# Performance work log

Hardware: AMD Instinct MI355X
Metric: run time of the kernel (lower is better)

## Reference

```python
import jax, jax.numpy as jnp
import numpy as np

N = 100000      # nodes
E = 1600000     # edges (avg degree 16)
F_IN = 64       # input features
HID = 16        # ChebConv hidden (fixed in source)
C = 40          # num_classes
K = 2           # Chebyshev order (fixed in source)
LAMBDA_MAX = 2.0  # PyG ChebConv default


def setup_inputs() -> dict:
    key = jax.random.key(0)
    ks = jax.random.split(key, 6)
    x = jax.random.normal(ks[0], (N, F_IN), dtype=jnp.float32)
    edge_index = jax.random.randint(ks[1], (2, E), 0, N, dtype=jnp.int32)
    edge_weight = jax.random.uniform(ks[2], (E,), dtype=jnp.float32)
    W1 = jax.random.normal(ks[3], (K, F_IN, HID), dtype=jnp.float32) / np.float32(np.sqrt(F_IN))
    b1 = jnp.zeros((HID,), dtype=jnp.float32)
    W2 = jax.random.normal(ks[4], (K, HID, C), dtype=jnp.float32) / np.float32(np.sqrt(HID))
    b2 = jnp.zeros((C,), dtype=jnp.float32)
    return {"x": x, "edge_weight": edge_weight, "W1": W1, "b1": b1,
            "W2": W2, "b2": b2, "edge_index": edge_index}


def _cheb_norm(src, dst, edge_weight):
    # deg from symmetric normalization (aggregate at dst, PyG col)
    deg = jax.ops.segment_sum(edge_weight, dst, num_segments=N)
    dinv = jnp.where(deg > 0, jax.lax.rsqrt(jnp.maximum(deg, 1e-30)), 0.0)
    # Lhat = 2L/lambda_max - I ; with L = I - A_norm -> edge weight = -(2/lmax)*A_norm
    norm = -(2.0 / LAMBDA_MAX) * dinv[src] * edge_weight * dinv[dst]
    loop = 2.0 / LAMBDA_MAX - 1.0  # self-loop weight (0 for lambda_max=2)
    return norm, loop


def _cheb_conv(x, src, dst, norm, loop, W, b):
    # K=2: Tx0 = x, Tx1 = Lhat @ x (sparse gather-scale-scatter)
    Tx1 = jax.ops.segment_sum(norm[:, None] * x[src], dst, num_segments=N) + loop * x
    return jnp.einsum('nf,fo->no', x, W[0]) + jnp.einsum('nf,fo->no', Tx1, W[1]) + b


def reference(x, edge_weight, W1, b1, W2, b2, edge_index):
    src, dst = edge_index[0], edge_index[1]
    norm, loop = _cheb_norm(src, dst, edge_weight)
    h = jax.nn.relu(_cheb_conv(x, src, dst, norm, loop, W1, b1))
    # F.dropout with training=False is identity (inference reference)
    o = _cheb_conv(h, src, dst, norm, loop, W2, b2)
    return jax.nn.log_softmax(o, axis=1)
```

## Files before the change

### kernel.cpp

```cpp
#include <hip/hip_runtime.h>
#include <math.h>

#define NN 100000
#define NE 1600000
#define FIN 64
#define HID 16
#define NC 40

#define NG 512
#define GN 196
#define GCAP 3600
#define CH 4096
#define NBK ((NE + CH - 1) / CH)

typedef unsigned int u32;
typedef unsigned long long u64;
typedef unsigned short u16;

__device__ inline u16 f2bf(float f) {
    u32 u = __float_as_uint(f);
    return (u16)((u + 0x7FFF + ((u >> 16) & 1)) >> 16);
}
__device__ inline float bf2f(u16 v) { return __uint_as_float(((u32)v) << 16); }

__global__ void k_zero(int* __restrict__ p) {
    p[blockIdx.x * 256 + threadIdx.x] = 0;
}

__global__ void __launch_bounds__(256) k_bucket(const int* __restrict__ src,
                                                const int* __restrict__ dst,
                                                const float* __restrict__ ew,
                                                int* __restrict__ bcur,
                                                u64* __restrict__ stg) {
    __shared__ u64 stage[CH];
    __shared__ int lcnt[NG];
    __shared__ int loff[NG];
    __shared__ int lcur[NG];
    __shared__ int gst[NG];
    __shared__ int ssum[256];
    __shared__ int totsh;
    int tid = threadIdx.x;
    int e0 = blockIdx.x * CH;
    for (int i = tid; i < NG; i += 256) lcnt[i] = 0;
    __syncthreads();
    u32 hb[16];
    #pragma unroll
    for (int k = 0; k < 16; ++k) {
        int e = e0 + k * 256 + tid;
        hb[k] = 0xFFFFFFFFu;
        if (e < NE) {
            int d = dst[e];
            int g = d / GN;
            hb[k] = ((u32)g << 16) | (u32)(d - g * GN);
            atomicAdd(&lcnt[g], 1);
        }
    }
    __syncthreads();
    int b0 = lcnt[2 * tid], b1c = lcnt[2 * tid + 1];
    int s = b0 + b1c;
    ssum[tid] = s;
    __syncthreads();
    #pragma unroll
    for (int off = 1; off < 256; off <<= 1) {
        int t = tid >= off ? ssum[tid - off] : 0;
        __syncthreads();
        ssum[tid] += t;
        __syncthreads();
    }
    int excl = ssum[tid] - s;
    loff[2 * tid] = excl;         loff[2 * tid + 1] = excl + b0;
    lcur[2 * tid] = excl;         lcur[2 * tid + 1] = excl + b0;
    gst[2 * tid]     = atomicAdd(&bcur[(2 * tid) << 4], b0);
    gst[2 * tid + 1] = atomicAdd(&bcur[(2 * tid + 1) << 4], b1c);
    if (tid == 255) totsh = ssum[255];
    __syncthreads();
    #pragma unroll
    for (int k = 0; k < 16; ++k) {
        if (hb[k] != 0xFFFFFFFFu) {
            int e = e0 + k * 256 + tid;
            int g = hb[k] >> 16;
            u32 q = (u32)fminf(ew[e] * 32767.f + 0.5f, 32767.f);
            u32 lo = (u32)src[e] | (q << 17);
            int slot = atomicAdd(&lcur[g], 1);
            stage[slot] = ((u64)hb[k] << 32) | (u64)lo;
        }
    }
    __syncthreads();
    int total = totsh;
    for (int i = tid; i < total; i += 256) {
        u64 r = stage[i];
        int g = (int)(r >> 48);
        int slot = gst[g] + (i - loff[g]);
        if (slot < GCAP) stg[(size_t)g * GCAP + slot] = r;
    }
}

__global__ void __launch_bounds__(256) k_build(const u64* __restrict__ stg,
                                               const int* __restrict__ bcur,
                                               int* __restrict__ row_ptr,
                                               float* __restrict__ dinv,
                                               u32* __restrict__ edges4) {
    __shared__ u32 hc[GN];
    __shared__ u32 hw[GN];
    __shared__ int tsum[256];
    __shared__ int sb[NG];
    int g = blockIdx.x, tid = threadIdx.x;
    for (int i = tid; i < GN; i += 256) { hc[i] = 0; hw[i] = 0; }
    for (int i = tid; i < NG; i += 256) sb[i] = bcur[i << 4];
    __syncthreads();
    int n = sb[g];
    int b0 = sb[2 * tid], b1 = sb[2 * tid + 1];
    const u64* base = stg + (size_t)g * GCAP;
    for (int i = tid; i < n; i += 256) {
        u64 r = base[i];
        int ld = (int)((r >> 32) & 0xFFFF);
        atomicAdd(&hc[ld], 1u);
        atomicAdd(&hw[ld], ((u32)r) >> 17);
    }
    __syncthreads();
    int s2 = b0 + b1;
    tsum[tid] = s2;
    __syncthreads();
    #pragma unroll
    for (int off = 1; off < 256; off <<= 1) {
        int t = tid >= off ? tsum[tid - off] : 0;
        __syncthreads();
        tsum[tid] += t;
        __syncthreads();
    }
    int excl = tsum[tid] - s2;
    sb[2 * tid] = excl; sb[2 * tid + 1] = excl + b0;
    __syncthreads();
    int gbase = sb[g];
    int c = (tid < GN) ? (int)hc[tid] : 0;
    tsum[tid] = c;
    __syncthreads();
    #pragma unroll
    for (int off = 1; off < 256; off <<= 1) {
        int t = tid >= off ? tsum[tid - off] : 0;
        __syncthreads();
        tsum[tid] += t;
        __syncthreads();
    }
    if (tid < GN) {
        int run = gbase + tsum[tid] - c;
        int nd = g * GN + tid;
        if (nd <= NN) {
            row_ptr[nd] = run;
            if (nd < NN) {
                float deg = (float)hw[tid] * (1.0f / 32767.0f);
                dinv[nd] = deg > 0.f ? rsqrtf(fmaxf(deg, 1e-30f)) : 0.f;
            }
        }
        hc[tid] = (u32)run;
    }
    __syncthreads();
    for (int i = tid; i < n; i += 256) {
        u64 r = base[i];
        int ld = (int)((r >> 32) & 0xFFFF);
        edges4[atomicAdd(&hc[ld], 1u)] = (u32)r;
    }
}

__global__ void __launch_bounds__(256) k_mm1(const float* __restrict__ x,
                                             const float* __restrict__ W1,
                                             const float* __restrict__ dinv,
                                             float* __restrict__ A1,
                                             u16* __restrict__ B0h) {
    __shared__ float4 w4[512];
    int tid = threadIdx.x;
    for (int i = tid; i < 512; i += 256) w4[i] = *(const float4*)(W1 + i * 4);
    __syncthreads();
    int sel = tid >> 7;
    int node = blockIdx.x * 128 + (tid & 127);
    if (node >= NN) return;
    const float4* xr = (const float4*)(x + node * FIN);
    const float4* wb = w4 + sel * 256;
    float4 a0 = {0,0,0,0}, a1 = {0,0,0,0}, a2 = {0,0,0,0}, a3 = {0,0,0,0};
    #pragma unroll
    for (int ft = 0; ft < 16; ++ft) {
        float4 xv = xr[ft];
        const float4* wf = wb + ft * 16;
        #pragma unroll
        for (int q = 0; q < 4; ++q) {
            float xs = q == 0 ? xv.x : q == 1 ? xv.y : q == 2 ? xv.z : xv.w;
            float4 w0 = wf[q * 4 + 0], w1v = wf[q * 4 + 1], w2v = wf[q * 4 + 2], w3v = wf[q * 4 + 3];
            a0.x += xs * w0.x; a0.y += xs * w0.y; a0.z += xs * w0.z; a0.w += xs * w0.w;
            a1.x += xs * w1v.x; a1.y += xs * w1v.y; a1.z += xs * w1v.z; a1.w += xs * w1v.w;
            a2.x += xs * w2v.x; a2.y += xs * w2v.y; a2.z += xs * w2v.z; a2.w += xs * w2v.w;
            a3.x += xs * w3v.x; a3.y += xs * w3v.y; a3.z += xs * w3v.z; a3.w += xs * w3v.w;
        }
    }
    if (sel == 0) {
        float4* o = (float4*)(A1 + node * HID);
        o[0] = a0; o[1] = a1; o[2] = a2; o[3] = a3;
    } else {
        float di = dinv[node];
        uint4 p0, p1;
        p0.x = f2bf(a0.x * di) | ((u32)f2bf(a0.y * di) << 16);
        p0.y = f2bf(a0.z * di) | ((u32)f2bf(a0.w * di) << 16);
        p0.z = f2bf(a1.x * di) | ((u32)f2bf(a1.y * di) << 16);
        p0.w = f2bf(a1.z * di) | ((u32)f2bf(a1.w * di) << 16);
        p1.x = f2bf(a2.x * di) | ((u32)f2bf(a2.y * di) << 16);
        p1.y = f2bf(a2.z * di) | ((u32)f2bf(a2.w * di) << 16);
        p1.z = f2bf(a3.x * di) | ((u32)f2bf(a3.y * di) << 16);
        p1.w = f2bf(a3.z * di) | ((u32)f2bf(a3.w * di) << 16);
        uint4* o = (uint4*)(B0h + node * HID);
        o[0] = p0; o[1] = p1;
    }
}

template <int MODE>
__global__ void k_gather(const int* __restrict__ row_ptr, const u32* __restrict__ edges4,
                         const u16* __restrict__ Bh,
                         const float* __restrict__ A1, const float* __restrict__ b1,
                         const float* __restrict__ dinv,
                         float* __restrict__ o1, u16* __restrict__ o2) {
    int node = blockIdx.x * 4 + (threadIdx.x >> 6);
    int lane = threadIdx.x & 63;
    int es = lane >> 4, j = lane & 15;
    if (node >= NN) return;
    int beg = row_ptr[node], end = row_ptr[node + 1];
    int p0 = beg + es;
    float acc = 0.f;
    if (end - beg <= 16) {
        u32 r[4];
        #pragma unroll
        for (int k = 0; k < 4; ++k) {
            int p = p0 + 4 * k;
            r[k] = (p < end) ? edges4[p] : 0u;
        }
        #pragma unroll
        for (int k = 0; k < 4; ++k)
            acc += (float)(r[k] >> 17) * bf2f(Bh[(r[k] & 0x1FFFF) * HID + j]);
    } else {
        u32 r[8];
        #pragma unroll
        for (int k = 0; k < 8; ++k) {
            int p = p0 + 4 * k;
            r[k] = (p < end) ? edges4[p] : 0u;
        }
        #pragma unroll
        for (int k = 0; k < 8; ++k)
            acc += (float)(r[k] >> 17) * bf2f(Bh[(r[k] & 0x1FFFF) * HID + j]);
        for (int p = p0 + 32; p < end; p += 4) {
            u32 rr = edges4[p];
            acc += (float)(rr >> 17) * bf2f(Bh[(rr & 0x1FFFF) * HID + j]);
        }
    }
    acc *= (1.0f / 32767.0f);
    acc += __shfl_xor(acc, 16, 64);
    acc += __shfl_xor(acc, 32, 64);
    if (es == 0) {
        float di = dinv[node];
        if (MODE == 0) {
            float v = A1[node * HID + j] - di * acc + b1[j];
            float hh = fmaxf(v, 0.f);
            o1[node * HID + j] = hh;
            o2[node * HID + j] = f2bf(hh * di);
        } else {
            o1[node * HID + j] = -di * acc;
        }
    }
}

__global__ void __launch_bounds__(256) k_mm2_lsm(const float* __restrict__ h,
                                                 const float* __restrict__ Th,
                                                 const float* __restrict__ W2,
                                                 const float* __restrict__ b2,
                                                 float* __restrict__ out) {
    __shared__ float4 w4[32][10];
    __shared__ float sb2[NC];
    int tid = threadIdx.x;
    for (int i = tid; i < 320; i += 256) {
        int f = i / 10, ct = i % 10;
        w4[f][ct] = *(const float4*)(W2 + f * 40 + ct * 4);
    }
    for (int i = tid; i < NC; i += 256) sb2[i] = b2[i];
    __syncthreads();
    int node = blockIdx.x * 256 + tid;
    if (node >= NN) return;
    float v[32];
    const float4* hp = (const float4*)(h + node * HID);
    const float4* tp = (const float4*)(Th + node * HID);
    #pragma unroll
    for (int q = 0; q < 4; ++q) {
        float4 a = hp[q];
        v[4 * q + 0] = a.x; v[4 * q + 1] = a.y; v[4 * q + 2] = a.z; v[4 * q + 3] = a.w;
        float4 b = tp[q];
        v[16 + 4 * q + 0] = b.x; v[16 + 4 * q + 1] = b.y; v[16 + 4 * q + 2] = b.z; v[16 + 4 * q + 3] = b.w;
    }
    float lg[NC];
    #pragma unroll
    for (int ct = 0; ct < 10; ++ct) {
        float ax = sb2[ct * 4 + 0], ay = sb2[ct * 4 + 1], az = sb2[ct * 4 + 2], aw = sb2[ct * 4 + 3];
        #pragma unroll
        for (int f = 0; f < 32; ++f) {
            float4 wv = w4[f][ct];
            ax += v[f] * wv.x; ay += v[f] * wv.y; az += v[f] * wv.z; aw += v[f] * wv.w;
        }
        lg[ct * 4 + 0] = ax; lg[ct * 4 + 1] = ay; lg[ct * 4 + 2] = az; lg[ct * 4 + 3] = aw;
    }
    float m = lg[0];
    #pragma unroll
    for (int c = 1; c < NC; ++c) m = fmaxf(m, lg[c]);
    float sum = 0.f;
    #pragma unroll
    for (int c = 0; c < NC; ++c) sum += __expf(lg[c] - m);
    float lse = m + __logf(sum);
    float* orow = out + node * NC;
    #pragma unroll
    for (int ct = 0; ct < 10; ++ct) {
        float4 r;
        r.x = lg[ct * 4 + 0] - lse; r.y = lg[ct * 4 + 1] - lse;
        r.z = lg[ct * 4 + 2] - lse; r.w = lg[ct * 4 + 3] - lse;
        *(float4*)(orow + ct * 4) = r;
    }
}

extern "C" void kernel_launch(void* const* d_in, const int* in_sizes, int n_in,
                              void* d_out, int out_size, void* d_ws, size_t ws_size,
                              hipStream_t stream) {
    const float* x  = (const float*)d_in[0];
    const float* ew = (const float*)d_in[1];
    const float* W1 = (const float*)d_in[2];
    const float* b1 = (const float*)d_in[3];
    const float* W2 = (const float*)d_in[4];
    const float* b2 = (const float*)d_in[5];
    const int*   ei = (const int*)d_in[6];
    const int* src = ei;
    const int* dst = ei + NE;
    float* out = (float*)d_out;

    const int NPAD = 100352;
    int*   bcur    = (int*)d_ws;
    u64*   stg     = (u64*)(bcur + NG * 16);
    u32*   edges4  = (u32*)(stg + (size_t)NG * GCAP);
    int*   row_ptr = (int*)(edges4 + NE);
    float* dinv    = (float*)(row_ptr + NPAD);
    float* A1      = dinv + NPAD;
    float* h       = A1 + NN * HID;
    float* Th      = h + NN * HID;
    u16*   B0h     = (u16*)(Th + NN * HID);
    u16*   h2      = B0h + NN * HID;

    k_zero<<<NG * 16 / 256, 256, 0, stream>>>(bcur);
    k_bucket<<<NBK, 256, 0, stream>>>(src, dst, ew, bcur, stg);
    k_build<<<NG, 256, 0, stream>>>(stg, bcur, row_ptr, dinv, edges4);
    k_mm1<<<(NN + 127) / 128, 256, 0, stream>>>(x, W1, dinv, A1, B0h);
    k_gather<0><<<(NN + 3) / 4, 256, 0, stream>>>(row_ptr, edges4, B0h, A1, b1, dinv, h, h2);
    k_gather<1><<<(NN + 3) / 4, 256, 0, stream>>>(row_ptr, edges4, h2, nullptr, nullptr, dinv, Th, nullptr);
    k_mm2_lsm<<<(NN + 255) / 256, 256, 0, stream>>>(h, Th, W2, b2, out);
}
```

Measured before the change: 135.1 us.

## Rewrite SpMM gather as edge-parallel blocks with shared-memory atomic accumulation

The CSR gather kernels change from one wavefront per node to one block per 64-node group. Threads now iterate over all edges of the group, eight threads per edge with each loading a packed bf16 pair, and accumulate into shared memory with atomics keyed by a new per-edge local destination byte. The build kernel writes that byte. The aim is to balance load across nodes of uneven degree and remove idle lanes on low-degree nodes. The cost is an extra byte array written and read per edge, plus shared-memory atomic contention among edges that share a destination.

```diff
diff --git a/kernel.cpp b/kernel.cpp
--- a/kernel.cpp
+++ b/kernel.cpp
@@ -12,16 +12,18 @@
 #define GCAP 3600
 #define CH 4096
 #define NBK ((NE + CH - 1) / CH)
+#define GB 64
+#define NGB ((NN + GB - 1) / GB)
 
 typedef unsigned int u32;
 typedef unsigned long long u64;
 typedef unsigned short u16;
+typedef unsigned char u8;
 
 __device__ inline u16 f2bf(float f) {
     u32 u = __float_as_uint(f);
     return (u16)((u + 0x7FFF + ((u >> 16) & 1)) >> 16);
 }
-__device__ inline float bf2f(u16 v) { return __uint_as_float(((u32)v) << 16); }
 
 __global__ void k_zero(int* __restrict__ p) {
     p[blockIdx.x * 256 + threadIdx.x] = 0;
@@ -99,7 +101,8 @@
                                                const int* __restrict__ bcur,
                                                int* __restrict__ row_ptr,
                                                float* __restrict__ dinv,
-                                               u32* __restrict__ edges4) {
+                                               u32* __restrict__ edges4,
+                                               u8* __restrict__ dloc) {
     __shared__ u32 hc[GN];
     __shared__ u32 hw[GN];
     __shared__ int tsum[256];
@@ -158,7 +161,9 @@
     for (int i = tid; i < n; i += 256) {
         u64 r = base[i];
         int ld = (int)((r >> 32) & 0xFFFF);
-        edges4[atomicAdd(&hc[ld], 1u)] = (u32)r;
+        int pos = (int)atomicAdd(&hc[ld], 1u);
+        edges4[pos] = (u32)r;
+        dloc[pos] = (u8)((g * GN + ld) & 63);
     }
 }
 
@@ -211,55 +216,54 @@
 }
 
 template <int MODE>
-__global__ void k_gather(const int* __restrict__ row_ptr, const u32* __restrict__ edges4,
-                         const u16* __restrict__ Bh,
-                         const float* __restrict__ A1, const float* __restrict__ b1,
-                         const float* __restrict__ dinv,
-                         float* __restrict__ o1, u16* __restrict__ o2) {
-    int node = blockIdx.x * 4 + (threadIdx.x >> 6);
-    int lane = threadIdx.x & 63;
-    int es = lane >> 4, j = lane & 15;
-    if (node >= NN) return;
-    int beg = row_ptr[node], end = row_ptr[node + 1];
-    int p0 = beg + es;
-    float acc = 0.f;
-    if (end - beg <= 16) {
-        u32 r[4];
-        #pragma unroll
-        for (int k = 0; k < 4; ++k) {
-            int p = p0 + 4 * k;
-            r[k] = (p < end) ? edges4[p] : 0u;
-        }
-        #pragma unroll
-        for (int k = 0; k < 4; ++k)
-            acc += (float)(r[k] >> 17) * bf2f(Bh[(r[k] & 0x1FFFF) * HID + j]);
-    } else {
-        u32 r[8];
-        #pragma unroll
-        for (int k = 0; k < 8; ++k) {
-            int p = p0 + 4 * k;
-            r[k] = (p < end) ? edges4[p] : 0u;
-        }
-        #pragma unroll
-        for (int k = 0; k < 8; ++k)
-            acc += (float)(r[k] >> 17) * bf2f(Bh[(r[k] & 0x1FFFF) * HID + j]);
-        for (int p = p0 + 32; p < end; p += 4) {
-            u32 rr = edges4[p];
-            acc += (float)(rr >> 17) * bf2f(Bh[(rr & 0x1FFFF) * HID + j]);
-        }
-    }
-    acc *= (1.0f / 32767.0f);
-    acc += __shfl_xor(acc, 16, 64);
-    acc += __shfl_xor(acc, 32, 64);
-    if (es == 0) {
-        float di = dinv[node];
+__global__ void __launch_bounds__(256) k_gather(const int* __restrict__ row_ptr,
+                                                const u32* __restrict__ edges4,
+                                                const u8* __restrict__ dloc,
+                                                const u16* __restrict__ Bh,
+                                                const float* __restrict__ A1,
+                                                const float* __restrict__ b1,
+                                                const float* __restrict__ dinv,
+                                                float* __restrict__ o1,
+                                                u16* __restrict__ o2) {
+    __shared__ float acc[GB * HID];
+    int tid = threadIdx.x;
+    int n0 = blockIdx.x * GB;
+    #pragma unroll
+    for (int i = tid; i < GB * HID; i += 256) acc[i] = 0.f;
+    __syncthreads();
+    int nend = n0 + GB; if (nend > NN) nend = NN;
+    int beg = row_ptr[n0], end = row_ptr[nend];
+    const u32* Bw = (const u32*)Bh;
+    int total = (end - beg) << 3;
+    for (int i = tid; i < total; i += 256) {
+        int e = beg + (i >> 3);
+        int q = i & 7;
+        u32 rec = edges4[e];
+        u32 c = Bw[(rec & 0x1FFFF) * 8 + q];
+        float w = (float)(rec >> 17);
+        int dl = (int)dloc[e];
+        atomicAdd(&acc[dl * HID + 2 * q],     w * __uint_as_float(c << 16));
+        atomicAdd(&acc[dl * HID + 2 * q + 1], w * __uint_as_float(c & 0xFFFF0000u));
+    }
+    __syncthreads();
+    for (int idx = tid; idx < GB * 8; idx += 256) {
+        int ln = idx >> 3, q = idx & 7;
+        int nd = n0 + ln;
+        if (nd >= NN) continue;
+        float di = dinv[nd];
+        float sc = di * (1.0f / 32767.0f);
+        float aL = acc[ln * HID + 2 * q];
+        float aH = acc[ln * HID + 2 * q + 1];
+        int f = 2 * q;
         if (MODE == 0) {
-            float v = A1[node * HID + j] - di * acc + b1[j];
-            float hh = fmaxf(v, 0.f);
-            o1[node * HID + j] = hh;
-            o2[node * HID + j] = f2bf(hh * di);
+            float2 a = *(const float2*)(A1 + nd * HID + f);
+            float2 bb = *(const float2*)(b1 + f);
+            float hL = fmaxf(a.x - sc * aL + bb.x, 0.f);
+            float hH = fmaxf(a.y - sc * aH + bb.y, 0.f);
+            *(float2*)(o1 + nd * HID + f) = make_float2(hL, hH);
+            ((u32*)o2)[nd * 8 + q] = (u32)f2bf(hL * di) | ((u32)f2bf(hH * di) << 16);
         } else {
-            o1[node * HID + j] = -di * acc;
+            *(float2*)(o1 + nd * HID + f) = make_float2(-sc * aL, -sc * aH);
         }
     }
 }
@@ -343,12 +347,13 @@
     float* Th      = h + NN * HID;
     u16*   B0h     = (u16*)(Th + NN * HID);
     u16*   h2      = B0h + NN * HID;
+    u8*    dloc    = (u8*)(h2 + NN * HID);
 
     k_zero<<<NG * 16 / 256, 256, 0, stream>>>(bcur);
     k_bucket<<<NBK, 256, 0, stream>>>(src, dst, ew, bcur, stg);
-    k_build<<<NG, 256, 0, stream>>>(stg, bcur, row_ptr, dinv, edges4);
+    k_build<<<NG, 256, 0, stream>>>(stg, bcur, row_ptr, dinv, edges4, dloc);
     k_mm1<<<(NN + 127) / 128, 256, 0, stream>>>(x, W1, dinv, A1, B0h);
-    k_gather<0><<<(NN + 3) / 4, 256, 0, stream>>>(row_ptr, edges4, B0h, A1, b1, dinv, h, h2);
-    k_gather<1><<<(NN + 3) / 4, 256, 0, stream>>>(row_ptr, edges4, h2, nullptr, nullptr, dinv, Th, nullptr);
+    k_gather<0><<<NGB, 256, 0, stream>>>(row_ptr, edges4, dloc, B0h, A1, b1, dinv, h, h2);
+    k_gather<1><<<NGB, 256, 0, stream>>>(row_ptr, edges4, dloc, h2, nullptr, nullptr, dinv, Th, nullptr);
     k_mm2_lsm<<<(NN + 255) / 256, 256, 0, stream>>>(h, Th, W2, b2, out);
 }
```

After: 382.9 us. +183.5%, slower.
